# Optimization experiments

Hardware: AMD Instinct MI355X
Metric: run time of the kernel (lower is better)

## Reference

```python
import jax, jax.numpy as jnp
import numpy as np

N_NODES = 100000
N_EDGES = 1600000
D_IN = 128
D_OUT = 128
EPSILON = 0.0


def setup_inputs() -> dict:
    key = jax.random.key(0)
    k1, k2, k3, k4, k5 = jax.random.split(key, 5)
    indices = jax.random.randint(k1, (2, N_EDGES), 0, N_NODES, dtype=jnp.int64 if jax.config.jax_enable_x64 else jnp.int32)
    values = jax.random.uniform(k2, (N_EDGES,), dtype=jnp.float32)
    features = jax.random.normal(k3, (N_NODES, D_IN), dtype=jnp.float32)
    # Xavier-uniform linear weights, zero biases (as in init_parameters)
    lim1 = float(np.sqrt(6.0 / (D_IN + D_OUT)))
    lim2 = float(np.sqrt(6.0 / (D_OUT + D_OUT)))
    W1 = jax.random.uniform(k4, (D_IN, D_OUT), minval=-lim1, maxval=lim1, dtype=jnp.float32)
    W2 = jax.random.uniform(k5, (D_OUT, D_OUT), minval=-lim2, maxval=lim2, dtype=jnp.float32)
    b1 = jnp.zeros((D_OUT,), dtype=jnp.float32)
    b2 = jnp.zeros((D_OUT,), dtype=jnp.float32)
    return {"indices": indices, "values": values, "features": features,
            "W1": W1, "b1": b1, "W2": W2, "b2": b2}


def reference(indices, values, features, W1, b1, W2, b2):
    row, col = indices[0], indices[1]
    # SpMM: out[r] = sum_e values[e] * features[col[e]]  (sparse_adj @ features)
    messages = values[:, None] * features[col]              # [E, D_IN]
    neighbor = jax.ops.segment_sum(messages, row, num_segments=N_NODES)  # [N, D_IN]
    combined = (1.0 + EPSILON) * features + neighbor        # epsilon residual
    h = jax.nn.relu(combined @ W1 + b1)                     # Linear -> ReLU
    out = h @ W2 + b2                                       # Linear
    # dropout is identity in eval mode
    return out
```

## Files before the change

kernel.cpp:

```cpp
#include <hip/hip_runtime.h>

#define N_NODES 100000
#define N_EDGES 1600000
#define D 128
#define NB 782

typedef unsigned short u16;
typedef unsigned int u32;
typedef __attribute__((ext_vector_type(8))) short bf16x8;
typedef __attribute__((ext_vector_type(4))) float f32x4;

__device__ __forceinline__ u16 f2bf(float f) {
    u32 u = __float_as_uint(f);
    u += 0x7fffu + ((u >> 16) & 1u);
    return (u16)(u >> 16);
}


__global__ void convert_feat(const float4* __restrict__ f4, uint4* __restrict__ o4) {
    int idx = blockIdx.x * blockDim.x + threadIdx.x;
    float4 a = f4[idx * 2], b = f4[idx * 2 + 1];
    uint4 o;
    o.x = (u32)f2bf(a.x) | ((u32)f2bf(a.y) << 16);
    o.y = (u32)f2bf(a.z) | ((u32)f2bf(a.w) << 16);
    o.z = (u32)f2bf(b.x) | ((u32)f2bf(b.y) << 16);
    o.w = (u32)f2bf(b.z) | ((u32)f2bf(b.w) << 16);
    o4[idx] = o;
}

__global__ void convert_w(const float* __restrict__ W1, const float* __restrict__ W2,
                          u16* __restrict__ W1t, u16* __restrict__ W2t) {
    int flat = blockIdx.x * blockDim.x + threadIdx.x;
    int m = flat >> 14;
    int idx = flat & 16383;
    int n = idx & 127;
    int k = idx >> 7;
    const float* src = m ? W2 : W1;
    u16* dst = m ? W2t : W1t;
    dst[n * 128 + k] = f2bf(src[k * 128 + n]);
}


__global__ __launch_bounds__(256) void bucket_hist(const int* __restrict__ row,
                                                   int* __restrict__ bhist) {
    __shared__ int h[NB];
    int t = threadIdx.x;
    for (int i = t; i < NB; i += 256) h[i] = 0;
    __syncthreads();
    int base = blockIdx.x * 4096 + t;
#pragma unroll
    for (int i = 0; i < 16; ++i) {
        int e = base + i * 256;
        if (e < N_EDGES) atomicAdd(&h[row[e] >> 7], 1);
    }
    __syncthreads();
    for (int i = t; i < NB; i += 256) {
        int c = h[i];
        if (c) atomicAdd(&bhist[i], c);
    }
}

__global__ void bucket_scan(const int* __restrict__ bhist, int* __restrict__ bucketOff,
                            int* __restrict__ bucketCursor) {
    __shared__ int part[256];
    int t = threadIdx.x;
    int v[4];
    int s = 0;
#pragma unroll
    for (int i = 0; i < 4; ++i) {
        int idx = t * 4 + i;
        v[i] = (idx < NB) ? bhist[idx] : 0;
        s += v[i];
    }
    int mine = s;
    part[t] = s;
    __syncthreads();
    for (int d = 1; d < 256; d <<= 1) {
        int x = (t >= d) ? part[t - d] : 0;
        __syncthreads();
        part[t] += x;
        __syncthreads();
    }
    int run = part[t] - mine;
#pragma unroll
    for (int i = 0; i < 4; ++i) {
        int idx = t * 4 + i;
        if (idx < NB) {
            bucketOff[idx] = run;
            bucketCursor[idx] = run;
        }
        run += v[i];
    }
    if (t == 0) bucketOff[NB] = N_EDGES;
}

__global__ __launch_bounds__(256) void bin_pass(const int* __restrict__ row,
                                                const int* __restrict__ col,
                                                const float* __restrict__ val,
                                                int* __restrict__ bucketCursor,
                                                int2* __restrict__ binned) {
    __shared__ int hist[NB];
    __shared__ int lbase[NB];
    int t = threadIdx.x;
    for (int i = t; i < NB; i += 256) hist[i] = 0;
    __syncthreads();
    int base = blockIdx.x * 4096;
    int r[16];
#pragma unroll
    for (int i = 0; i < 16; ++i) {
        int e = base + i * 256 + t;
        r[i] = (e < N_EDGES) ? row[e] : -1;
        if (r[i] >= 0) atomicAdd(&hist[r[i] >> 7], 1);
    }
    __syncthreads();
    for (int i = t; i < NB; i += 256) {
        int c = hist[i];
        lbase[i] = c ? atomicAdd(&bucketCursor[i], c) : 0;
    }
    __syncthreads();
    for (int i = t; i < NB; i += 256) hist[i] = 0;
    __syncthreads();
#pragma unroll
    for (int i = 0; i < 16; ++i) {
        if (r[i] < 0) continue;
        int e = base + i * 256 + t;
        int bkt = r[i] >> 7;
        int pos = lbase[bkt] + atomicAdd(&hist[bkt], 1);
        int2 ev;
        ev.x = col[e] | ((r[i] & 127) << 17);
        ev.y = __float_as_int(val[e]);
        binned[pos] = ev;
    }
}

__global__ __launch_bounds__(256) void bucket_sort(const int2* __restrict__ binned,
                                                   const int* __restrict__ bucketOff,
                                                   int* __restrict__ offsets,
                                                   int2* __restrict__ scev) {
    __shared__ int h[128];
    __shared__ int cur[128];
    int b = blockIdx.x, t = threadIdx.x;
    int row0 = b << 7;
    int nrows = N_NODES - row0;
    if (nrows > 128) nrows = 128;
    if (t < 128) h[t] = 0;
    __syncthreads();
    int lo = bucketOff[b], hi = bucketOff[b + 1];
    for (int i = lo + t; i < hi; i += 256)
        atomicAdd(&h[((u32)binned[i].x) >> 17], 1);
    __syncthreads();
    if (t < 128) cur[t] = h[t];
    __syncthreads();
    for (int d = 1; d < 128; d <<= 1) {
        int x = 0;
        if (t < 128 && t >= d) x = cur[t - d];
        __syncthreads();
        if (t < 128) cur[t] += x;
        __syncthreads();
    }
    if (t < 128) {
        int excl = lo + cur[t] - h[t];
        if (t < nrows) offsets[row0 + t] = excl;
        cur[t] = excl;
    }
    __syncthreads();
    for (int i = lo + t; i < hi; i += 256) {
        int2 ev = binned[i];
        int rl = ((u32)ev.x) >> 17;
        int pos = atomicAdd(&cur[rl], 1);
        scev[pos] = make_int2(ev.x & 0x1FFFF, ev.y);
    }
    if (b == 0 && t == 0) offsets[N_NODES] = N_EDGES;
}


__global__ __launch_bounds__(256) void spmm_bf16(
    const int2* __restrict__ scev, const int* __restrict__ offsets,
    const u32* __restrict__ featb, u32* __restrict__ Xb) {
    int wid0 = (blockIdx.x * blockDim.x + threadIdx.x) >> 6;
    int wid = __builtin_amdgcn_readfirstlane(wid0);
    int lane = threadIdx.x & 63;
    if (wid >= N_NODES) return;
    int beg = offsets[wid], end = offsets[wid + 1];
    u32 self = featb[wid * 64 + lane];
    float ax0 = __uint_as_float(self << 16);
    float ay0 = __uint_as_float(self & 0xffff0000u);
    float ax1 = 0.f, ay1 = 0.f;
    int j = beg;
    for (; j + 8 <= end; j += 8) {
        int2 e[8];
        u32 p[8];
#pragma unroll
        for (int u = 0; u < 8; ++u) e[u] = scev[j + u];
#pragma unroll
        for (int u = 0; u < 8; ++u) p[u] = featb[e[u].x * 64 + lane];
#pragma unroll
        for (int u = 0; u < 8; ++u) {
            float v = __int_as_float(e[u].y);
            float lo = __uint_as_float(p[u] << 16);
            float hi = __uint_as_float(p[u] & 0xffff0000u);
            if (u & 1) {
                ax1 += v * lo;
                ay1 += v * hi;
            } else {
                ax0 += v * lo;
                ay0 += v * hi;
            }
        }
    }
    for (; j < end; ++j) {
        int2 e = scev[j];
        float v = __int_as_float(e.y);
        u32 p = featb[e.x * 64 + lane];
        ax0 += v * __uint_as_float(p << 16);
        ay0 += v * __uint_as_float(p & 0xffff0000u);
    }
    float accx = ax0 + ax1;
    float accy = ay0 + ay1;
    Xb[wid * 64 + lane] = (u32)f2bf(accx) | ((u32)f2bf(accy) << 16);
}


template <int RELU, int OUT32>
__global__ __launch_bounds__(256, 2) void gemm_mfma(
    const u16* __restrict__ Xb, const u16* __restrict__ Wt,
    const float* __restrict__ bias, u16* __restrict__ outb, float* __restrict__ outf) {
    __shared__ u16 Ws[128][136];
    int t = threadIdx.x;
    {
        const uint4* wsrc = (const uint4*)Wt;
#pragma unroll
        for (int i = 0; i < 8; ++i) {
            int f = t + 256 * i;
            int n = f >> 4;
            int c8 = (f & 15) << 3;
            *(uint4*)&Ws[n][c8] = wsrc[f];
        }
    }
    __syncthreads();

    int w = t >> 6, lane = t & 63;
    int quad = lane >> 4, l16 = lane & 15;
    int row0 = blockIdx.x * 128 + w * 32;

    f32x4 acc[2][8];
#pragma unroll
    for (int rt = 0; rt < 2; ++rt)
#pragma unroll
        for (int ct = 0; ct < 8; ++ct) acc[rt][ct] = (f32x4){0.f, 0.f, 0.f, 0.f};

    int ra = row0 + l16;
    int rb = row0 + 16 + l16;
    if (ra > N_NODES - 1) ra = N_NODES - 1;
    if (rb > N_NODES - 1) rb = N_NODES - 1;
    const u16* pa = Xb + (size_t)ra * D + quad * 8;
    const u16* pb = Xb + (size_t)rb * D + quad * 8;

#pragma unroll
    for (int kb = 0; kb < 128; kb += 32) {
        bf16x8 a0 = *(const bf16x8*)(pa + kb);
        bf16x8 a1 = *(const bf16x8*)(pb + kb);
#pragma unroll
        for (int ct = 0; ct < 8; ++ct) {
            bf16x8 b = *(const bf16x8*)&Ws[ct * 16 + l16][kb + quad * 8];
            acc[0][ct] = __builtin_amdgcn_mfma_f32_16x16x32_bf16(a0, b, acc[0][ct], 0, 0, 0);
            acc[1][ct] = __builtin_amdgcn_mfma_f32_16x16x32_bf16(a1, b, acc[1][ct], 0, 0, 0);
        }
    }

    float bv[8];
#pragma unroll
    for (int ct = 0; ct < 8; ++ct) bv[ct] = bias[ct * 16 + l16];

#pragma unroll
    for (int rt = 0; rt < 2; ++rt) {
#pragma unroll
        for (int r = 0; r < 4; ++r) {
            int row = row0 + rt * 16 + quad * 4 + r;
            if (row >= N_NODES) continue;
#pragma unroll
            for (int ct = 0; ct < 8; ++ct) {
                float v = acc[rt][ct][r] + bv[ct];
                if (RELU) v = fmaxf(v, 0.f);
                int col = ct * 16 + l16;
                if (OUT32) outf[(size_t)row * D + col] = v;
                else outb[(size_t)row * D + col] = f2bf(v);
            }
        }
    }
}

extern "C" void kernel_launch(void* const* d_in, const int* in_sizes, int n_in,
                              void* d_out, int out_size, void* d_ws, size_t ws_size,
                              hipStream_t stream) {
    const int* indices = (const int*)d_in[0];
    const float* values = (const float*)d_in[1];
    const float* features = (const float*)d_in[2];
    const float* W1 = (const float*)d_in[3];
    const float* b1 = (const float*)d_in[4];
    const float* W2 = (const float*)d_in[5];
    const float* b2 = (const float*)d_in[6];

    const int* row = indices;
    const int* col = indices + N_EDGES;

    int* wsI = (int*)d_ws;
    int* offsets = wsI;
    int* bhist = wsI + N_NODES + 8;
    int* bucketOff = bhist + NB;
    int* bucketCursor = bucketOff + NB + 1;
    int2* scev = (int2*)(bucketCursor + NB + 7);
    u16* featb = (u16*)(scev + N_EDGES);
    u16* Hb = featb;
    u16* W1t = featb + (size_t)N_NODES * D;
    u16* W2t = W1t + 16384;

    int2* binned = (int2*)d_out;
    u16* Xb = (u16*)((char*)d_out + (size_t)N_NODES * D * 2);
    float* outf = (float*)d_out;

    hipMemsetAsync(bhist, 0, NB * sizeof(int), stream);

    convert_feat<<<N_NODES * D / 8 / 256, 256, 0, stream>>>((const float4*)features, (uint4*)featb);
    convert_w<<<128, 256, 0, stream>>>(W1, W2, W1t, W2t);

    int cb = (N_EDGES + 4095) / 4096;
    bucket_hist<<<cb, 256, 0, stream>>>(row, bhist);
    bucket_scan<<<1, 256, 0, stream>>>(bhist, bucketOff, bucketCursor);
    bin_pass<<<cb, 256, 0, stream>>>(row, col, values, bucketCursor, binned);
    bucket_sort<<<NB, 256, 0, stream>>>(binned, bucketOff, offsets, scev);

    spmm_bf16<<<(N_NODES * 64 + 255) / 256, 256, 0, stream>>>(scev, offsets, (const u32*)featb,
                                                              (u32*)Xb);

    int gb = (N_NODES + 127) / 128;
    gemm_mfma<1, 0><<<gb, 256, 0, stream>>>(Xb, W1t, b1, Hb, nullptr);
    gemm_mfma<0, 1><<<gb, 256, 0, stream>>>(Hb, W2t, b2, nullptr, outf);
}
```

Measured before the change: 312.6 us.

## Use fixed-capacity row buckets to drop histogram and scan passes

```diff
diff --git a/kernel.cpp b/kernel.cpp
--- a/kernel.cpp
+++ b/kernel.cpp
@@ -4,6 +4,7 @@
 #define N_EDGES 1600000
 #define D 128
 #define NB 782
+#define BCAP 2560
 
 typedef unsigned short u16;
 typedef unsigned int u32;
@@ -41,63 +42,10 @@
 }
 
 
-__global__ __launch_bounds__(256) void bucket_hist(const int* __restrict__ row,
-                                                   int* __restrict__ bhist) {
-    __shared__ int h[NB];
-    int t = threadIdx.x;
-    for (int i = t; i < NB; i += 256) h[i] = 0;
-    __syncthreads();
-    int base = blockIdx.x * 4096 + t;
-#pragma unroll
-    for (int i = 0; i < 16; ++i) {
-        int e = base + i * 256;
-        if (e < N_EDGES) atomicAdd(&h[row[e] >> 7], 1);
-    }
-    __syncthreads();
-    for (int i = t; i < NB; i += 256) {
-        int c = h[i];
-        if (c) atomicAdd(&bhist[i], c);
-    }
-}
-
-__global__ void bucket_scan(const int* __restrict__ bhist, int* __restrict__ bucketOff,
-                            int* __restrict__ bucketCursor) {
-    __shared__ int part[256];
-    int t = threadIdx.x;
-    int v[4];
-    int s = 0;
-#pragma unroll
-    for (int i = 0; i < 4; ++i) {
-        int idx = t * 4 + i;
-        v[i] = (idx < NB) ? bhist[idx] : 0;
-        s += v[i];
-    }
-    int mine = s;
-    part[t] = s;
-    __syncthreads();
-    for (int d = 1; d < 256; d <<= 1) {
-        int x = (t >= d) ? part[t - d] : 0;
-        __syncthreads();
-        part[t] += x;
-        __syncthreads();
-    }
-    int run = part[t] - mine;
-#pragma unroll
-    for (int i = 0; i < 4; ++i) {
-        int idx = t * 4 + i;
-        if (idx < NB) {
-            bucketOff[idx] = run;
-            bucketCursor[idx] = run;
-        }
-        run += v[i];
-    }
-    if (t == 0) bucketOff[NB] = N_EDGES;
-}
-
 __global__ __launch_bounds__(256) void bin_pass(const int* __restrict__ row,
                                                 const int* __restrict__ col,
                                                 const float* __restrict__ val,
-                                                int* __restrict__ bucketCursor,
+                                                int* __restrict__ bucketCount,
                                                 int2* __restrict__ binned) {
     __shared__ int hist[NB];
     __shared__ int lbase[NB];
@@ -115,7 +63,7 @@
     __syncthreads();
     for (int i = t; i < NB; i += 256) {
         int c = hist[i];
-        lbase[i] = c ? atomicAdd(&bucketCursor[i], c) : 0;
+        lbase[i] = c ? atomicAdd(&bucketCount[i], c) : 0;
     }
     __syncthreads();
     for (int i = t; i < NB; i += 256) hist[i] = 0;
@@ -125,7 +73,7 @@
         if (r[i] < 0) continue;
         int e = base + i * 256 + t;
         int bkt = r[i] >> 7;
-        int pos = lbase[bkt] + atomicAdd(&hist[bkt], 1);
+        int pos = bkt * BCAP + lbase[bkt] + atomicAdd(&hist[bkt], 1);
         int2 ev;
         ev.x = col[e] | ((r[i] & 127) << 17);
         ev.y = __float_as_int(val[e]);
@@ -134,8 +82,8 @@
 }
 
 __global__ __launch_bounds__(256) void bucket_sort(const int2* __restrict__ binned,
-                                                   const int* __restrict__ bucketOff,
-                                                   int* __restrict__ offsets,
+                                                   const int* __restrict__ bucketCount,
+                                                   int2* __restrict__ rowRange,
                                                    int2* __restrict__ scev) {
     __shared__ int h[128];
     __shared__ int cur[128];
@@ -145,7 +93,8 @@
     if (nrows > 128) nrows = 128;
     if (t < 128) h[t] = 0;
     __syncthreads();
-    int lo = bucketOff[b], hi = bucketOff[b + 1];
+    int lo = b * BCAP;
+    int hi = lo + bucketCount[b];
     for (int i = lo + t; i < hi; i += 256)
         atomicAdd(&h[((u32)binned[i].x) >> 17], 1);
     __syncthreads();
@@ -160,7 +109,7 @@
     }
     if (t < 128) {
         int excl = lo + cur[t] - h[t];
-        if (t < nrows) offsets[row0 + t] = excl;
+        if (t < nrows) rowRange[row0 + t] = make_int2(excl, excl + h[t]);
         cur[t] = excl;
     }
     __syncthreads();
@@ -170,32 +119,31 @@
         int pos = atomicAdd(&cur[rl], 1);
         scev[pos] = make_int2(ev.x & 0x1FFFF, ev.y);
     }
-    if (b == 0 && t == 0) offsets[N_NODES] = N_EDGES;
 }
 
 
 __global__ __launch_bounds__(256) void spmm_bf16(
-    const int2* __restrict__ scev, const int* __restrict__ offsets,
+    const int2* __restrict__ scev, const int2* __restrict__ rowRange,
     const u32* __restrict__ featb, u32* __restrict__ Xb) {
     int wid0 = (blockIdx.x * blockDim.x + threadIdx.x) >> 6;
     int wid = __builtin_amdgcn_readfirstlane(wid0);
     int lane = threadIdx.x & 63;
     if (wid >= N_NODES) return;
-    int beg = offsets[wid], end = offsets[wid + 1];
+    int2 rr = rowRange[wid];
+    int j = rr.x, end = rr.y;
     u32 self = featb[wid * 64 + lane];
     float ax0 = __uint_as_float(self << 16);
     float ay0 = __uint_as_float(self & 0xffff0000u);
     float ax1 = 0.f, ay1 = 0.f;
-    int j = beg;
-    for (; j + 8 <= end; j += 8) {
-        int2 e[8];
-        u32 p[8];
-#pragma unroll
-        for (int u = 0; u < 8; ++u) e[u] = scev[j + u];
-#pragma unroll
-        for (int u = 0; u < 8; ++u) p[u] = featb[e[u].x * 64 + lane];
-#pragma unroll
-        for (int u = 0; u < 8; ++u) {
+    for (; j + 16 <= end; j += 16) {
+        int2 e[16];
+        u32 p[16];
+#pragma unroll
+        for (int u = 0; u < 16; ++u) e[u] = scev[j + u];
+#pragma unroll
+        for (int u = 0; u < 16; ++u) p[u] = featb[e[u].x * 64 + lane];
+#pragma unroll
+        for (int u = 0; u < 16; ++u) {
             float v = __int_as_float(e[u].y);
             float lo = __uint_as_float(p[u] << 16);
             float hi = __uint_as_float(p[u] & 0xffff0000u);
@@ -208,6 +156,27 @@
             }
         }
     }
+    for (; j + 4 <= end; j += 4) {
+        int2 e[4];
+        u32 p[4];
+#pragma unroll
+        for (int u = 0; u < 4; ++u) e[u] = scev[j + u];
+#pragma unroll
+        for (int u = 0; u < 4; ++u) p[u] = featb[e[u].x * 64 + lane];
+#pragma unroll
+        for (int u = 0; u < 4; ++u) {
+            float v = __int_as_float(e[u].y);
+            float lo = __uint_as_float(p[u] << 16);
+            float hi = __uint_as_float(p[u] & 0xffff0000u);
+            if (u & 1) {
+                ax1 += v * lo;
+                ay1 += v * hi;
+            } else {
+                ax0 += v * lo;
+                ay0 += v * hi;
+            }
+        }
+    }
     for (; j < end; ++j) {
         int2 e = scev[j];
         float v = __int_as_float(e.y);
@@ -305,35 +274,30 @@
     const int* col = indices + N_EDGES;
 
     int* wsI = (int*)d_ws;
-    int* offsets = wsI;
-    int* bhist = wsI + N_NODES + 8;
-    int* bucketOff = bhist + NB;
-    int* bucketCursor = bucketOff + NB + 1;
-    int2* scev = (int2*)(bucketCursor + NB + 7);
-    u16* featb = (u16*)(scev + N_EDGES);
-    u16* Hb = featb;
-    u16* W1t = featb + (size_t)N_NODES * D;
+    int* bucketCount = wsI;
+    int2* rowRange = (int2*)(wsI + 784);
+    int2* scev = (int2*)(wsI + 784 + 2 * N_NODES);
+    u32* featb = (u32*)(wsI + 784 + 2 * N_NODES + 2 * NB * BCAP);
+    u16* Hb = (u16*)featb;
+    u16* W1t = (u16*)(featb + (size_t)N_NODES * 64);
     u16* W2t = W1t + 16384;
 
     int2* binned = (int2*)d_out;
-    u16* Xb = (u16*)((char*)d_out + (size_t)N_NODES * D * 2);
+    u32* Xb = (u32*)((char*)d_out + (size_t)N_NODES * D * 2);
     float* outf = (float*)d_out;
 
-    hipMemsetAsync(bhist, 0, NB * sizeof(int), stream);
+    hipMemsetAsync(bucketCount, 0, NB * sizeof(int), stream);
 
     convert_feat<<<N_NODES * D / 8 / 256, 256, 0, stream>>>((const float4*)features, (uint4*)featb);
     convert_w<<<128, 256, 0, stream>>>(W1, W2, W1t, W2t);
 
     int cb = (N_EDGES + 4095) / 4096;
-    bucket_hist<<<cb, 256, 0, stream>>>(row, bhist);
-    bucket_scan<<<1, 256, 0, stream>>>(bhist, bucketOff, bucketCursor);
-    bin_pass<<<cb, 256, 0, stream>>>(row, col, values, bucketCursor, binned);
-    bucket_sort<<<NB, 256, 0, stream>>>(binned, bucketOff, offsets, scev);
-
-    spmm_bf16<<<(N_NODES * 64 + 255) / 256, 256, 0, stream>>>(scev, offsets, (const u32*)featb,
-                                                              (u32*)Xb);
+    bin_pass<<<cb, 256, 0, stream>>>(row, col, values, bucketCount, binned);
+    bucket_sort<<<NB, 256, 0, stream>>>(binned, bucketCount, rowRange, scev);
+
+    spmm_bf16<<<(N_NODES * 64 + 255) / 256, 256, 0, stream>>>(scev, rowRange, featb, Xb);
 
     int gb = (N_NODES + 127) / 128;
-    gemm_mfma<1, 0><<<gb, 256, 0, stream>>>(Xb, W1t, b1, Hb, nullptr);
+    gemm_mfma<1, 0><<<gb, 256, 0, stream>>>((const u16*)Xb, W1t, b1, Hb, nullptr);
     gemm_mfma<0, 1><<<gb, 256, 0, stream>>>(Hb, W2t, b2, nullptr, outf);
 }
```

Result: faster. 289.4 us (-7.4%).
